# Kernel optimization log

Hardware: AMD Instinct MI355X
Metric: run time of the kernel (lower is better)

The kernel has to match this reference:

```python
import jax, jax.numpy as jnp
import numpy as np

D = 8196        # 4*n_landmark + (n_agents-1)*size_channel + 4
H = 4096        # hidden_size
MLP_HID = 32
OUT = 2 + 128   # 2 + size_channel


def setup_inputs() -> dict:
    key = jax.random.key(0)
    ks = jax.random.split(key, 8)
    s = 0.02
    return {
        "x": jax.random.normal(ks[0], (D,), jnp.float32),
        "h0": jnp.zeros((H,), jnp.float32),
        "c0": jnp.zeros((H,), jnp.float32),
        # LSTM params (PyTorch layout: gates stacked as [i, f, g, o])
        "W_ih": jax.random.normal(ks[1], (4 * H, D), jnp.float32) * s,
        "W_hh": jax.random.normal(ks[2], (4 * H, H), jnp.float32) * s,
        "b_ih": jax.random.normal(ks[3], (4 * H,), jnp.float32) * s,
        "b_hh": jax.random.normal(ks[4], (4 * H,), jnp.float32) * s,
        # MLP: Linear(H,32) -> ReLU -> Linear(32, OUT) -> Sigmoid
        "W1": jax.random.normal(ks[5], (MLP_HID, H), jnp.float32) * s,
        "b1": jnp.zeros((MLP_HID,), jnp.float32),
        "W2": jax.random.normal(ks[6], (OUT, MLP_HID), jnp.float32) * s,
        "b2": jnp.zeros((OUT,), jnp.float32),
    }


def reference(x, h0, c0, W_ih, W_hh, b_ih, b_hh, W1, b1, W2, b2):
    # single LSTM step (batch=1, seq=1), PyTorch gate order i,f,g,o
    gates = W_ih @ x + b_ih + W_hh @ h0 + b_hh            # [4H]
    i, f, g, o = jnp.split(gates, 4)
    i = jax.nn.sigmoid(i)
    f = jax.nn.sigmoid(f)
    g = jnp.tanh(g)
    o = jax.nn.sigmoid(o)
    c = f * c0 + i * g
    h = o * jnp.tanh(c)                                   # [H]
    # MLP head: Linear -> ReLU -> Linear -> Sigmoid, then flatten
    z = jax.nn.relu(W1 @ h + b1)                          # [32]
    out = jax.nn.sigmoid(W2 @ z + b2)                     # [OUT]
    return out
```

## Files before the change

### kernel.cpp

```cpp
#include <hip/hip_runtime.h>
#include <hip/hip_bf16.h>

#define D 8196
#define H 4096
#define MLP_HID 32
#define OUT_N 130

__device__ __forceinline__ float sigmoidf_(float v) {
    return 1.0f / (1.0f + expf(-v));
}

__device__ __forceinline__ float dot4(float4 a, float4 b) {
    return a.x * b.x + a.y * b.y + a.z * b.z + a.w * b.w;
}

__device__ __forceinline__ float wave_reduce(float acc) {
    #pragma unroll
    for (int off = 32; off > 0; off >>= 1)
        acc += __shfl_down(acc, off);
    return acc;
}

__global__ __launch_bounds__(256) void lstm_step_kernel(
    const float* __restrict__ x, const float* __restrict__ h0,
    const float* __restrict__ c0,
    const float* __restrict__ W_ih, const float* __restrict__ W_hh,
    const float* __restrict__ b_ih, const float* __restrict__ b_hh,
    float* __restrict__ h_out)
{
    const int j    = blockIdx.x;
    const int wave = threadIdx.x >> 6;
    const int lane = threadIdx.x & 63;
    const int row  = wave * H + j;

    float acc = 0.0f;

    {
        const float4* __restrict__ Wr = (const float4*)(W_ih + (size_t)row * D);
        const float4* __restrict__ x4 = (const float4*)x;
        for (int idx = lane; idx < D / 4; idx += 64)
            acc += dot4(Wr[idx], x4[idx]);
    }
    {
        const float4* __restrict__ Wr = (const float4*)(W_hh + (size_t)row * H);
        const float4* __restrict__ h4 = (const float4*)h0;
        #pragma unroll 4
        for (int idx = lane; idx < H / 4; idx += 64)
            acc += dot4(Wr[idx], h4[idx]);
    }

    acc = wave_reduce(acc);

    __shared__ float gate[4];
    if (lane == 0)
        gate[wave] = acc + b_ih[row] + b_hh[row];
    __syncthreads();

    if (threadIdx.x == 0) {
        float ig = sigmoidf_(gate[0]);
        float fg = sigmoidf_(gate[1]);
        float gg = tanhf(gate[2]);
        float og = sigmoidf_(gate[3]);
        float c  = fg * c0[j] + ig * gg;
        h_out[j] = og * tanhf(c);
    }
}

__global__ __launch_bounds__(1024) void mlp_head_kernel(
    const float* __restrict__ h,
    const float* __restrict__ W1, const float* __restrict__ b1,
    const float* __restrict__ W2, const float* __restrict__ b2,
    float* __restrict__ out)
{
    __shared__ float z[MLP_HID];
    const int wave = threadIdx.x >> 6;
    const int lane = threadIdx.x & 63;

    for (int r = wave; r < MLP_HID; r += 16) {
        const float4* __restrict__ Wr = (const float4*)(W1 + (size_t)r * H);
        const float4* __restrict__ h4 = (const float4*)h;
        float acc = 0.0f;
        #pragma unroll 4
        for (int idx = lane; idx < H / 4; idx += 64)
            acc += dot4(Wr[idx], h4[idx]);
        acc = wave_reduce(acc);
        if (lane == 0)
            z[r] = fmaxf(acc + b1[r], 0.0f);
    }
    __syncthreads();

    const int t = threadIdx.x;
    if (t < OUT_N) {
        float acc = b2[t];
        #pragma unroll
        for (int k = 0; k < MLP_HID; ++k)
            acc += W2[t * MLP_HID + k] * z[k];
        out[t] = sigmoidf_(acc);
    }
}

extern "C" void kernel_launch(void* const* d_in, const int* in_sizes, int n_in,
                              void* d_out, int out_size, void* d_ws, size_t ws_size,
                              hipStream_t stream) {
    const float* x    = (const float*)d_in[0];
    const float* h0   = (const float*)d_in[1];
    const float* c0   = (const float*)d_in[2];
    const float* W_ih = (const float*)d_in[3];
    const float* W_hh = (const float*)d_in[4];
    const float* b_ih = (const float*)d_in[5];
    const float* b_hh = (const float*)d_in[6];
    const float* W1   = (const float*)d_in[7];
    const float* b1   = (const float*)d_in[8];
    const float* W2   = (const float*)d_in[9];
    const float* b2   = (const float*)d_in[10];
    float* out = (float*)d_out;

    float* h_ws = (float*)d_ws;

    lstm_step_kernel<<<H, 256, 0, stream>>>(x, h0, c0, W_ih, W_hh, b_ih, b_hh, h_ws);
    mlp_head_kernel<<<1, 1024, 0, stream>>>(h_ws, W1, b1, W2, b2, out);
}
```

Baseline: 166.5 us.

## Fuse LSTM step and MLP head via last-block atomic counter

Result: slower. 545.4 us (+227.5%).

```diff
diff --git a/kernel.cpp b/kernel.cpp
--- a/kernel.cpp
+++ b/kernel.cpp
@@ -6,11 +6,13 @@
 #define MLP_HID 32
 #define OUT_N 130
 
+typedef float vfloat4 __attribute__((ext_vector_type(4)));
+
 __device__ __forceinline__ float sigmoidf_(float v) {
     return 1.0f / (1.0f + expf(-v));
 }
 
-__device__ __forceinline__ float dot4(float4 a, float4 b) {
+__device__ __forceinline__ float dot4v(vfloat4 a, vfloat4 b) {
     return a.x * b.x + a.y * b.y + a.z * b.z + a.w * b.w;
 }
 
@@ -21,81 +23,106 @@
     return acc;
 }
 
-__global__ __launch_bounds__(256) void lstm_step_kernel(
+__global__ __launch_bounds__(256) void brain_fused_kernel(
     const float* __restrict__ x, const float* __restrict__ h0,
     const float* __restrict__ c0,
     const float* __restrict__ W_ih, const float* __restrict__ W_hh,
     const float* __restrict__ b_ih, const float* __restrict__ b_hh,
-    float* __restrict__ h_out)
+    const float* __restrict__ W1, const float* __restrict__ b1,
+    const float* __restrict__ W2, const float* __restrict__ b2,
+    float* __restrict__ out,
+    unsigned int* __restrict__ counter, float* __restrict__ h_ws)
 {
-    const int j    = blockIdx.x;
-    const int wave = threadIdx.x >> 6;
+    const int g    = threadIdx.x >> 6;
     const int lane = threadIdx.x & 63;
-    const int row  = wave * H + j;
+    const int j0   = blockIdx.x * 2;
+    const size_t r0 = (size_t)g * H + j0;
 
-    float acc = 0.0f;
+    float acc0 = 0.0f, acc1 = 0.0f;
 
     {
-        const float4* __restrict__ Wr = (const float4*)(W_ih + (size_t)row * D);
-        const float4* __restrict__ x4 = (const float4*)x;
-        for (int idx = lane; idx < D / 4; idx += 64)
-            acc += dot4(Wr[idx], x4[idx]);
+        const vfloat4* __restrict__ A0 = (const vfloat4*)(W_ih + r0 * D);
+        const vfloat4* __restrict__ A1 = (const vfloat4*)(W_ih + (r0 + 1) * D);
+        const vfloat4* __restrict__ x4 = (const vfloat4*)x;
+        #pragma unroll 4
+        for (int it = 0; it < 32; ++it) {
+            const int idx = it * 64 + lane;
+            const vfloat4 xv = x4[idx];
+            acc0 += dot4v(__builtin_nontemporal_load(&A0[idx]), xv);
+            acc1 += dot4v(__builtin_nontemporal_load(&A1[idx]), xv);
+        }
+        if (lane == 0) {
+            const vfloat4 xv = x4[2048];
+            acc0 += dot4v(__builtin_nontemporal_load(&A0[2048]), xv);
+            acc1 += dot4v(__builtin_nontemporal_load(&A1[2048]), xv);
+        }
     }
     {
-        const float4* __restrict__ Wr = (const float4*)(W_hh + (size_t)row * H);
-        const float4* __restrict__ h4 = (const float4*)h0;
+        const vfloat4* __restrict__ B0 = (const vfloat4*)(W_hh + r0 * H);
+        const vfloat4* __restrict__ B1 = (const vfloat4*)(W_hh + (r0 + 1) * H);
+        const vfloat4* __restrict__ h4 = (const vfloat4*)h0;
         #pragma unroll 4
-        for (int idx = lane; idx < H / 4; idx += 64)
-            acc += dot4(Wr[idx], h4[idx]);
+        for (int it = 0; it < 16; ++it) {
+            const int idx = it * 64 + lane;
+            const vfloat4 hv = h4[idx];
+            acc0 += dot4v(__builtin_nontemporal_load(&B0[idx]), hv);
+            acc1 += dot4v(__builtin_nontemporal_load(&B1[idx]), hv);
+        }
     }
 
-    acc = wave_reduce(acc);
+    acc0 = wave_reduce(acc0);
+    acc1 = wave_reduce(acc1);
 
-    __shared__ float gate[4];
-    if (lane == 0)
-        gate[wave] = acc + b_ih[row] + b_hh[row];
-    __syncthreads();
-
-    if (threadIdx.x == 0) {
-        float ig = sigmoidf_(gate[0]);
-        float fg = sigmoidf_(gate[1]);
-        float gg = tanhf(gate[2]);
-        float og = sigmoidf_(gate[3]);
-        float c  = fg * c0[j] + ig * gg;
-        h_out[j] = og * tanhf(c);
-    }
-}
-
-__global__ __launch_bounds__(1024) void mlp_head_kernel(
-    const float* __restrict__ h,
-    const float* __restrict__ W1, const float* __restrict__ b1,
-    const float* __restrict__ W2, const float* __restrict__ b2,
-    float* __restrict__ out)
-{
-    __shared__ float z[MLP_HID];
-    const int wave = threadIdx.x >> 6;
-    const int lane = threadIdx.x & 63;
-
-    for (int r = wave; r < MLP_HID; r += 16) {
-        const float4* __restrict__ Wr = (const float4*)(W1 + (size_t)r * H);
-        const float4* __restrict__ h4 = (const float4*)h;
-        float acc = 0.0f;
-        #pragma unroll 4
-        for (int idx = lane; idx < H / 4; idx += 64)
-            acc += dot4(Wr[idx], h4[idx]);
-        acc = wave_reduce(acc);
-        if (lane == 0)
-            z[r] = fmaxf(acc + b1[r], 0.0f);
+    __shared__ float gate[4][2];
+    __shared__ int lastflag;
+    if (lane == 0) {
+        gate[g][0] = acc0 + b_ih[r0]     + b_hh[r0];
+        gate[g][1] = acc1 + b_ih[r0 + 1] + b_hh[r0 + 1];
     }
     __syncthreads();
 
-    const int t = threadIdx.x;
-    if (t < OUT_N) {
-        float acc = b2[t];
+    if (threadIdx.x < 2) {
+        const int t = threadIdx.x;
+        const int j = j0 + t;
+        const float ig = sigmoidf_(gate[0][t]);
+        const float fg = sigmoidf_(gate[1][t]);
+        const float gg = tanhf(gate[2][t]);
+        const float og = sigmoidf_(gate[3][t]);
+        const float c  = fg * c0[j] + ig * gg;
+        h_ws[j] = og * tanhf(c);
+    }
+
+    __threadfence();
+    if (threadIdx.x == 0)
+        lastflag = (atomicAdd(counter, 1u) == (unsigned)(gridDim.x - 1));
+    __syncthreads();
+    if (!lastflag) return;
+    __threadfence();
+
+    __shared__ float z[MLP_HID];
+    {
+        const vfloat4* __restrict__ h4 = (const vfloat4*)h_ws;
+        for (int r = g; r < MLP_HID; r += 4) {
+            const vfloat4* __restrict__ Wr = (const vfloat4*)(W1 + (size_t)r * H);
+            float acc = 0.0f;
+            #pragma unroll 4
+            for (int it = 0; it < 16; ++it) {
+                const int idx = it * 64 + lane;
+                acc += dot4v(Wr[idx], h4[idx]);
+            }
+            acc = wave_reduce(acc);
+            if (lane == 0)
+                z[r] = fmaxf(acc + b1[r], 0.0f);
+        }
+    }
+    __syncthreads();
+
+    if (threadIdx.x < OUT_N) {
+        float acc = b2[threadIdx.x];
         #pragma unroll
         for (int k = 0; k < MLP_HID; ++k)
-            acc += W2[t * MLP_HID + k] * z[k];
-        out[t] = sigmoidf_(acc);
+            acc += W2[threadIdx.x * MLP_HID + k] * z[k];
+        out[threadIdx.x] = sigmoidf_(acc);
     }
 }
 
@@ -115,8 +142,10 @@
     const float* b2   = (const float*)d_in[10];
     float* out = (float*)d_out;
 
-    float* h_ws = (float*)d_ws;
+    unsigned int* counter = (unsigned int*)d_ws;
+    float* h_ws = (float*)((char*)d_ws + 256);
 
-    lstm_step_kernel<<<H, 256, 0, stream>>>(x, h0, c0, W_ih, W_hh, b_ih, b_hh, h_ws);
-    mlp_head_kernel<<<1, 1024, 0, stream>>>(h_ws, W1, b1, W2, b2, out);
+    (void)hipMemsetAsync(counter, 0, sizeof(unsigned int), stream);
+    brain_fused_kernel<<<H / 2, 256, 0, stream>>>(
+        x, h0, c0, W_ih, W_hh, b_ih, b_hh, W1, b1, W2, b2, out, counter, h_ws);
 }
```

## Stage x and h in shared memory and compute two hidden units per block

Applied to the files above, without the earlier changes.

Result: faster. 162.7 us (-2.3%).

```diff
diff --git a/kernel.cpp b/kernel.cpp
--- a/kernel.cpp
+++ b/kernel.cpp
@@ -5,6 +5,8 @@
 #define H 4096
 #define MLP_HID 32
 #define OUT_N 130
+#define ND4 2049
+#define NH4 1024
 
 __device__ __forceinline__ float sigmoidf_(float v) {
     return 1.0f / (1.0f + expf(-v));
@@ -21,47 +23,67 @@
     return acc;
 }
 
-__global__ __launch_bounds__(256) void lstm_step_kernel(
+__global__ __launch_bounds__(256, 3) void lstm_step_kernel(
     const float* __restrict__ x, const float* __restrict__ h0,
     const float* __restrict__ c0,
     const float* __restrict__ W_ih, const float* __restrict__ W_hh,
     const float* __restrict__ b_ih, const float* __restrict__ b_hh,
     float* __restrict__ h_out)
 {
-    const int j    = blockIdx.x;
-    const int wave = threadIdx.x >> 6;
-    const int lane = threadIdx.x & 63;
-    const int row  = wave * H + j;
+    __shared__ float4 xs[ND4];
+    __shared__ float4 hs[NH4];
+    __shared__ float gate[4][2];
 
-    float acc = 0.0f;
-
+    const int tid = threadIdx.x;
     {
-        const float4* __restrict__ Wr = (const float4*)(W_ih + (size_t)row * D);
         const float4* __restrict__ x4 = (const float4*)x;
-        for (int idx = lane; idx < D / 4; idx += 64)
-            acc += dot4(Wr[idx], x4[idx]);
+        const float4* __restrict__ h4 = (const float4*)h0;
+        for (int i = tid; i < ND4; i += 256) xs[i] = x4[i];
+        for (int i = tid; i < NH4; i += 256) hs[i] = h4[i];
     }
-    {
-        const float4* __restrict__ Wr = (const float4*)(W_hh + (size_t)row * H);
-        const float4* __restrict__ h4 = (const float4*)h0;
-        #pragma unroll 4
-        for (int idx = lane; idx < H / 4; idx += 64)
-            acc += dot4(Wr[idx], h4[idx]);
-    }
-
-    acc = wave_reduce(acc);
-
-    __shared__ float gate[4];
-    if (lane == 0)
-        gate[wave] = acc + b_ih[row] + b_hh[row];
     __syncthreads();
 
-    if (threadIdx.x == 0) {
-        float ig = sigmoidf_(gate[0]);
-        float fg = sigmoidf_(gate[1]);
-        float gg = tanhf(gate[2]);
-        float og = sigmoidf_(gate[3]);
-        float c  = fg * c0[j] + ig * gg;
+    const int g    = tid >> 6;
+    const int lane = tid & 63;
+    const int j0   = blockIdx.x * 2;
+
+    #pragma unroll
+    for (int rr = 0; rr < 2; ++rr) {
+        const size_t r = (size_t)g * H + j0 + rr;
+        float a = 0.0f;
+
+        {
+            const float4* __restrict__ A = (const float4*)(W_ih + r * D);
+            #pragma unroll 8
+            for (int it = 0; it < 32; ++it) {
+                const int idx = it * 64 + lane;
+                a += dot4(A[idx], xs[idx]);
+            }
+            if (lane == 0)
+                a += dot4(A[2048], xs[2048]);
+        }
+        {
+            const float4* __restrict__ B = (const float4*)(W_hh + r * H);
+            #pragma unroll 8
+            for (int it = 0; it < 16; ++it) {
+                const int idx = it * 64 + lane;
+                a += dot4(B[idx], hs[idx]);
+            }
+        }
+
+        a = wave_reduce(a);
+        if (lane == 0)
+            gate[g][rr] = a + b_ih[r] + b_hh[r];
+    }
+    __syncthreads();
+
+    if (tid < 2) {
+        const int j = j0 + tid;
+        const float ig = sigmoidf_(gate[0][tid]);
+        const float fg = sigmoidf_(gate[1][tid]);
+        const float gg = tanhf(gate[2][tid]);
+        const float og = sigmoidf_(gate[3][tid]);
+        const float c  = fg * c0[j] + ig * gg;
         h_out[j] = og * tanhf(c);
     }
 }
@@ -117,6 +139,6 @@
 
     float* h_ws = (float*)d_ws;
 
-    lstm_step_kernel<<<H, 256, 0, stream>>>(x, h0, c0, W_ih, W_hh, b_ih, b_hh, h_ws);
+    lstm_step_kernel<<<H / 2, 256, 0, stream>>>(x, h0, c0, W_ih, W_hh, b_ih, b_hh, h_ws);
     mlp_head_kernel<<<1, 1024, 0, stream>>>(h_ws, W1, b1, W2, b2, out);
 }
```
